# Kernel optimization log

Measured on AMD Instinct MI355X. Metric: run time of the kernel, lower is better.

## Reference

```python
import jax, jax.numpy as jnp
import numpy as np

INFEATURES = 4096
OUTFEATURES = 11008
GROUP_SIZE = 128
N_GROUPS = INFEATURES // GROUP_SIZE  # 32
PACK = 8  # 32 bits / 4 bits


def _unpack_int4(packed):
    # packed: [R, C//8] int32 -> [R, C] int32 nibbles in [0, 15]
    shifts = (jnp.arange(PACK, dtype=jnp.int32) * 4)
    nib = (packed[:, :, None] >> shifts[None, None, :]) & 0xF
    return nib.reshape(packed.shape[0], packed.shape[1] * PACK)


def setup_inputs() -> dict:
    key = jax.random.key(0)
    k1, k2, k3, k4, k5 = jax.random.split(key, 5)
    x = jax.random.normal(k1, (2048, INFEATURES), dtype=jnp.float32)
    qweight = jax.random.randint(k2, (INFEATURES, OUTFEATURES // PACK), 0, 2147483647, dtype=jnp.int32)
    qzeros = jax.random.randint(k3, (N_GROUPS, OUTFEATURES // PACK), 0, 2147483647, dtype=jnp.int32)
    scales = jax.random.uniform(k4, (N_GROUPS, OUTFEATURES), minval=0.001, maxval=0.01, dtype=jnp.float32)
    bias = jax.random.normal(k5, (OUTFEATURES,), dtype=jnp.float32) * 0.01
    return {"x": x, "qweight": qweight, "qzeros": qzeros, "scales": scales, "bias": bias}


def reference(x, qweight, qzeros, scales, bias):
    # convert_from_uint4: dequantize packed int4 weight with per-group scale/zero
    w_int = _unpack_int4(qweight)                       # [in, out] int4 values
    z_int = _unpack_int4(qzeros)                        # [n_groups, out]
    dt = scales.dtype
    # broadcast group params to per-row (trivial g_idx: row i -> group i // GROUP_SIZE)
    z = jnp.repeat(z_int.astype(dt), GROUP_SIZE, axis=0)      # [in, out]
    s = jnp.repeat(scales, GROUP_SIZE, axis=0)                # [in, out]
    weight = (w_int.astype(dt) - z) * s                       # [in, out]
    out = jnp.matmul(x, weight) + bias                        # [tokens, out]
    return out
```

## Files before the change

kernel.cpp:

```cpp
#include <hip/hip_runtime.h>

typedef __bf16 bf16_t;
typedef bf16_t bf16x8 __attribute__((ext_vector_type(8)));
typedef float  floatx4 __attribute__((ext_vector_type(4)));
typedef unsigned int uint;

constexpr int Mdim = 2048;
constexpr int Kdim = 4096;
constexpr int Ndim = 11008;
constexpr int NPK  = Ndim / 8;
constexpr int BM = 128, BN = 128, BK = 64;
constexpr int SA = 72;
constexpr int SB = 72;
constexpr int SQ = 68;

__global__ void xcast_kernel(const float* __restrict__ x, bf16_t* __restrict__ xb)
{
    const int i = (blockIdx.x * 256 + threadIdx.x) * 8;
    const float4 a = *(const float4*)(x + i);
    const float4 b = *(const float4*)(x + i + 4);
    bf16x8 v;
    v[0] = (bf16_t)a.x; v[1] = (bf16_t)a.y; v[2] = (bf16_t)a.z; v[3] = (bf16_t)a.w;
    v[4] = (bf16_t)b.x; v[5] = (bf16_t)b.y; v[6] = (bf16_t)b.z; v[7] = (bf16_t)b.w;
    *(bf16x8*)(xb + i) = v;
}

template <bool PRE>
__global__ __launch_bounds__(256, 3)
void qgemm_kernel(const float* __restrict__ x,
                  const bf16_t* __restrict__ xb,
                  const uint* __restrict__ qweight,
                  const uint* __restrict__ qzeros,
                  const float* __restrict__ scales,
                  const float* __restrict__ bias,
                  float* __restrict__ out)
{
    __shared__ bf16_t As[BM * SA];
    __shared__ bf16_t Bs[BN * SB];
    __shared__ uint   qbuf[16 * SQ];

    const int t  = threadIdx.x;
    const int m0 = blockIdx.y * BM;
    const int n0 = blockIdx.x * BN;
    const int c0 = n0 >> 3;

    const int wave = t >> 6;
    const int lane = t & 63;
    const int quad = lane >> 4;
    const int l16  = lane & 15;
    const int mw = (wave >> 1) * 64;
    const int nw = (wave & 1) * 64;

    floatx4 acc[4][4];
#pragma unroll
    for (int i = 0; i < 4; ++i)
#pragma unroll
        for (int j = 0; j < 4; ++j)
            acc[i][j] = (floatx4){0.f, 0.f, 0.f, 0.f};

    const int am = t >> 3;
    const int ao = t & 7;
    const int qk  = t >> 2;
    const int qc4 = (t & 3) * 4;
    const int nloc  = t & 127;
    const int khalf = t >> 7;
    const int cc    = nloc >> 3;
    const int jsh   = (nloc & 7) * 4;

    for (int kt = 0; kt < Kdim / BK; ++kt) {
        const int k0 = kt * BK;
        const int g  = k0 >> 7;

#pragma unroll
        for (int p = 0; p < 4; ++p) {
            const int m = p * 32 + am;
            if (PRE) {
                const bf16x8 v = *(const bf16x8*)(xb + (size_t)(m0 + m) * Kdim + k0 + ao * 8);
                *(bf16x8*)&As[m * SA + ao * 8] = v;
            } else {
                const float* src = x + (size_t)(m0 + m) * Kdim + k0 + ao * 8;
                const float4 a = *(const float4*)src;
                const float4 b = *(const float4*)(src + 4);
                bf16x8 v;
                v[0] = (bf16_t)a.x; v[1] = (bf16_t)a.y; v[2] = (bf16_t)a.z; v[3] = (bf16_t)a.w;
                v[4] = (bf16_t)b.x; v[5] = (bf16_t)b.y; v[6] = (bf16_t)b.z; v[7] = (bf16_t)b.w;
                *(bf16x8*)&As[m * SA + ao * 8] = v;
            }
        }
        {
            const uint4 w4 = *(const uint4*)(qweight + (size_t)(k0 + qk) * NPK + c0 + qc4);
            qbuf[(qc4 + 0) * SQ + qk] = w4.x;
            qbuf[(qc4 + 1) * SQ + qk] = w4.y;
            qbuf[(qc4 + 2) * SQ + qk] = w4.z;
            qbuf[(qc4 + 3) * SQ + qk] = w4.w;
        }
        __syncthreads();

        {
            const uint  zw = qzeros[(size_t)g * NPK + c0 + cc];
            const float s  = scales[(size_t)g * Ndim + n0 + nloc];
            const float zs = (float)((zw >> jsh) & 15u) * s;
            const uint* qrow = &qbuf[cc * SQ + khalf * 32];
#pragma unroll
            for (int j = 0; j < 4; ++j) {
                const uint4 qa = *(const uint4*)(qrow + j * 8);
                const uint4 qb = *(const uint4*)(qrow + j * 8 + 4);
                bf16x8 v;
                v[0] = (bf16_t)((float)((qa.x >> jsh) & 15u) * s - zs);
                v[1] = (bf16_t)((float)((qa.y >> jsh) & 15u) * s - zs);
                v[2] = (bf16_t)((float)((qa.z >> jsh) & 15u) * s - zs);
                v[3] = (bf16_t)((float)((qa.w >> jsh) & 15u) * s - zs);
                v[4] = (bf16_t)((float)((qb.x >> jsh) & 15u) * s - zs);
                v[5] = (bf16_t)((float)((qb.y >> jsh) & 15u) * s - zs);
                v[6] = (bf16_t)((float)((qb.z >> jsh) & 15u) * s - zs);
                v[7] = (bf16_t)((float)((qb.w >> jsh) & 15u) * s - zs);
                *(bf16x8*)&Bs[nloc * SB + khalf * 32 + j * 8] = v;
            }
        }
        __syncthreads();

#pragma unroll
        for (int s = 0; s < 2; ++s) {
            bf16x8 fa[4], fb[4];
#pragma unroll
            for (int mt = 0; mt < 4; ++mt)
                fa[mt] = *(const bf16x8*)&As[(mw + mt * 16 + l16) * SA + s * 32 + quad * 8];
#pragma unroll
            for (int nt = 0; nt < 4; ++nt)
                fb[nt] = *(const bf16x8*)&Bs[(nw + nt * 16 + l16) * SB + s * 32 + quad * 8];
#pragma unroll
            for (int mt = 0; mt < 4; ++mt)
#pragma unroll
                for (int nt = 0; nt < 4; ++nt)
                    acc[mt][nt] = __builtin_amdgcn_mfma_f32_16x16x32_bf16(fa[mt], fb[nt], acc[mt][nt], 0, 0, 0);
        }
        __syncthreads();
    }

#pragma unroll
    for (int nt = 0; nt < 4; ++nt) {
        const int col = n0 + nw + nt * 16 + l16;
        const float b = bias[col];
#pragma unroll
        for (int mt = 0; mt < 4; ++mt) {
#pragma unroll
            for (int r = 0; r < 4; ++r) {
                const int row = m0 + mw + mt * 16 + quad * 4 + r;
                out[(size_t)row * Ndim + col] = acc[mt][nt][r] + b;
            }
        }
    }
}

extern "C" void kernel_launch(void* const* d_in, const int* in_sizes, int n_in,
                              void* d_out, int out_size, void* d_ws, size_t ws_size,
                              hipStream_t stream)
{
    const float* x        = (const float*)d_in[0];
    const uint*  qweight  = (const uint*)d_in[1];
    const uint*  qzeros   = (const uint*)d_in[2];
    const float* scales   = (const float*)d_in[3];
    const float* bias     = (const float*)d_in[4];
    float*       out      = (float*)d_out;
    bf16_t*      xb       = (bf16_t*)d_ws;

    const size_t xb_bytes = (size_t)Mdim * Kdim * sizeof(bf16_t);
    dim3 grid(Ndim / BN, Mdim / BM);

    if (ws_size >= xb_bytes) {
        xcast_kernel<<<(Mdim * Kdim) / (256 * 8), 256, 0, stream>>>(x, xb);
        qgemm_kernel<true><<<grid, dim3(256), 0, stream>>>(x, xb, qweight, qzeros, scales, bias, out);
    } else {
        qgemm_kernel<false><<<grid, dim3(256), 0, stream>>>(x, xb, qweight, qzeros, scales, bias, out);
    }
}
```

Before: 398.8 us.

## Dequantize weights directly into MFMA fragments and load A via global_load_lds

Removes the Bs shared-memory tile: each wave now dequantizes int4 weights from the packed qbuf straight into B fragment registers, which drops one LDS store/load round trip and one barrier per K step. Scales and zeros are hoisted to once per 128-row group, with two 64-wide halves processed inside. The A tile is loaded with global_load_lds (direct global-to-LDS) into an XOR-swizzled unpadded layout to avoid bank conflicts. In exchange, dequant work is duplicated across the two waves that share each N slice, and register pressure rises.

```diff
diff --git a/kernel.cpp b/kernel.cpp
--- a/kernel.cpp
+++ b/kernel.cpp
@@ -10,8 +10,6 @@
 constexpr int Ndim = 11008;
 constexpr int NPK  = Ndim / 8;
 constexpr int BM = 128, BN = 128, BK = 64;
-constexpr int SA = 72;
-constexpr int SB = 72;
 constexpr int SQ = 68;
 
 __global__ void xcast_kernel(const float* __restrict__ x, bf16_t* __restrict__ xb)
@@ -23,6 +21,12 @@
     v[0] = (bf16_t)a.x; v[1] = (bf16_t)a.y; v[2] = (bf16_t)a.z; v[3] = (bf16_t)a.w;
     v[4] = (bf16_t)b.x; v[5] = (bf16_t)b.y; v[6] = (bf16_t)b.z; v[7] = (bf16_t)b.w;
     *(bf16x8*)(xb + i) = v;
+}
+
+__device__ __forceinline__ void gload_lds16(const bf16_t* g, bf16_t* l)
+{
+    __builtin_amdgcn_global_load_lds((const __attribute__((address_space(1))) void*)g,
+                                     (__attribute__((address_space(3))) void*)l, 16, 0, 0);
 }
 
 template <bool PRE>
@@ -35,8 +39,7 @@
                   const float* __restrict__ bias,
                   float* __restrict__ out)
 {
-    __shared__ bf16_t As[BM * SA];
-    __shared__ bf16_t Bs[BN * SB];
+    __shared__ bf16_t As[BM * BK];
     __shared__ uint   qbuf[16 * SQ];
 
     const int t  = threadIdx.x;
@@ -51,6 +54,30 @@
     const int mw = (wave >> 1) * 64;
     const int nw = (wave & 1) * 64;
 
+    const int r8   = lane >> 3;
+    const int gs   = lane & 7;
+    const int gcol = gs ^ r8;
+
+    const int qk  = t >> 2;
+    const int qc4 = (t & 3) * 4;
+
+    const int jsh = (l16 & 7) * 4;
+    const int e3  = l16 & 7;
+    int qrowoff[4];
+#pragma unroll
+    for (int nt = 0; nt < 4; ++nt)
+        qrowoff[nt] = ((nw >> 3) + nt * 2 + (l16 >> 3)) * SQ;
+    int arowoff[4];
+#pragma unroll
+    for (int mt = 0; mt < 4; ++mt)
+        arowoff[mt] = (mw + mt * 16 + l16) * BK;
+    int aslot[2], qoff[2];
+#pragma unroll
+    for (int s2 = 0; s2 < 2; ++s2) {
+        aslot[s2] = (((s2 * 4 + quad) ^ e3) * 8);
+        qoff[s2]  = s2 * 32 + quad * 8;
+    }
+
     floatx4 acc[4][4];
 #pragma unroll
     for (int i = 0; i < 4; ++i)
@@ -58,83 +85,81 @@
         for (int j = 0; j < 4; ++j)
             acc[i][j] = (floatx4){0.f, 0.f, 0.f, 0.f};
 
-    const int am = t >> 3;
-    const int ao = t & 7;
-    const int qk  = t >> 2;
-    const int qc4 = (t & 3) * 4;
-    const int nloc  = t & 127;
-    const int khalf = t >> 7;
-    const int cc    = nloc >> 3;
-    const int jsh   = (nloc & 7) * 4;
-
-    for (int kt = 0; kt < Kdim / BK; ++kt) {
-        const int k0 = kt * BK;
-        const int g  = k0 >> 7;
-
-#pragma unroll
-        for (int p = 0; p < 4; ++p) {
-            const int m = p * 32 + am;
+    for (int g = 0; g < 32; ++g) {
+        float sN[4], zsN[4];
+#pragma unroll
+        for (int nt = 0; nt < 4; ++nt) {
+            const int col = n0 + nw + nt * 16 + l16;
+            const float sv = scales[(size_t)g * Ndim + col];
+            const uint  zw = qzeros[(size_t)g * NPK + (col >> 3)];
+            sN[nt]  = sv;
+            zsN[nt] = (float)((zw >> jsh) & 15u) * sv;
+        }
+
+#pragma unroll 1
+        for (int half = 0; half < 2; ++half) {
+            const int k0 = g * 128 + half * 64;
+
             if (PRE) {
-                const bf16x8 v = *(const bf16x8*)(xb + (size_t)(m0 + m) * Kdim + k0 + ao * 8);
-                *(bf16x8*)&As[m * SA + ao * 8] = v;
+#pragma unroll
+                for (int p = 0; p < 4; ++p) {
+                    const bf16_t* gp = xb + (size_t)(m0 + p * 32 + wave * 8 + r8) * Kdim
+                                          + k0 + gcol * 8;
+                    gload_lds16(gp, &As[(p * 32 + wave * 8) * BK]);
+                }
             } else {
-                const float* src = x + (size_t)(m0 + m) * Kdim + k0 + ao * 8;
-                const float4 a = *(const float4*)src;
-                const float4 b = *(const float4*)(src + 4);
-                bf16x8 v;
-                v[0] = (bf16_t)a.x; v[1] = (bf16_t)a.y; v[2] = (bf16_t)a.z; v[3] = (bf16_t)a.w;
-                v[4] = (bf16_t)b.x; v[5] = (bf16_t)b.y; v[6] = (bf16_t)b.z; v[7] = (bf16_t)b.w;
-                *(bf16x8*)&As[m * SA + ao * 8] = v;
-            }
+#pragma unroll
+                for (int p = 0; p < 4; ++p) {
+                    const int row = p * 32 + wave * 8 + r8;
+                    const float* src = x + (size_t)(m0 + row) * Kdim + k0 + gcol * 8;
+                    const float4 a = *(const float4*)src;
+                    const float4 b = *(const float4*)(src + 4);
+                    bf16x8 v;
+                    v[0] = (bf16_t)a.x; v[1] = (bf16_t)a.y; v[2] = (bf16_t)a.z; v[3] = (bf16_t)a.w;
+                    v[4] = (bf16_t)b.x; v[5] = (bf16_t)b.y; v[6] = (bf16_t)b.z; v[7] = (bf16_t)b.w;
+                    *(bf16x8*)&As[row * BK + gs * 8] = v;
+                }
+            }
+
+            {
+                const uint4 w4 = *(const uint4*)(qweight + (size_t)(k0 + qk) * NPK + c0 + qc4);
+                qbuf[(qc4 + 0) * SQ + qk] = w4.x;
+                qbuf[(qc4 + 1) * SQ + qk] = w4.y;
+                qbuf[(qc4 + 2) * SQ + qk] = w4.z;
+                qbuf[(qc4 + 3) * SQ + qk] = w4.w;
+            }
+            __syncthreads();
+
+#pragma unroll
+            for (int s2 = 0; s2 < 2; ++s2) {
+                bf16x8 fa[4], fb[4];
+#pragma unroll
+                for (int mt = 0; mt < 4; ++mt)
+                    fa[mt] = *(const bf16x8*)&As[arowoff[mt] + aslot[s2]];
+#pragma unroll
+                for (int nt = 0; nt < 4; ++nt) {
+                    const uint* qr = &qbuf[qrowoff[nt] + qoff[s2]];
+                    const uint4 qa = *(const uint4*)qr;
+                    const uint4 qb = *(const uint4*)(qr + 4);
+                    bf16x8 v;
+                    v[0] = (bf16_t)((float)((qa.x >> jsh) & 15u) * sN[nt] - zsN[nt]);
+                    v[1] = (bf16_t)((float)((qa.y >> jsh) & 15u) * sN[nt] - zsN[nt]);
+                    v[2] = (bf16_t)((float)((qa.z >> jsh) & 15u) * sN[nt] - zsN[nt]);
+                    v[3] = (bf16_t)((float)((qa.w >> jsh) & 15u) * sN[nt] - zsN[nt]);
+                    v[4] = (bf16_t)((float)((qb.x >> jsh) & 15u) * sN[nt] - zsN[nt]);
+                    v[5] = (bf16_t)((float)((qb.y >> jsh) & 15u) * sN[nt] - zsN[nt]);
+                    v[6] = (bf16_t)((float)((qb.z >> jsh) & 15u) * sN[nt] - zsN[nt]);
+                    v[7] = (bf16_t)((float)((qb.w >> jsh) & 15u) * sN[nt] - zsN[nt]);
+                    fb[nt] = v;
+                }
+#pragma unroll
+                for (int mt = 0; mt < 4; ++mt)
+#pragma unroll
+                    for (int nt = 0; nt < 4; ++nt)
+                        acc[mt][nt] = __builtin_amdgcn_mfma_f32_16x16x32_bf16(fa[mt], fb[nt], acc[mt][nt], 0, 0, 0);
+            }
+            __syncthreads();
         }
-        {
-            const uint4 w4 = *(const uint4*)(qweight + (size_t)(k0 + qk) * NPK + c0 + qc4);
-            qbuf[(qc4 + 0) * SQ + qk] = w4.x;
-            qbuf[(qc4 + 1) * SQ + qk] = w4.y;
-            qbuf[(qc4 + 2) * SQ + qk] = w4.z;
-            qbuf[(qc4 + 3) * SQ + qk] = w4.w;
-        }
-        __syncthreads();
-
-        {
-            const uint  zw = qzeros[(size_t)g * NPK + c0 + cc];
-            const float s  = scales[(size_t)g * Ndim + n0 + nloc];
-            const float zs = (float)((zw >> jsh) & 15u) * s;
-            const uint* qrow = &qbuf[cc * SQ + khalf * 32];
-#pragma unroll
-            for (int j = 0; j < 4; ++j) {
-                const uint4 qa = *(const uint4*)(qrow + j * 8);
-                const uint4 qb = *(const uint4*)(qrow + j * 8 + 4);
-                bf16x8 v;
-                v[0] = (bf16_t)((float)((qa.x >> jsh) & 15u) * s - zs);
-                v[1] = (bf16_t)((float)((qa.y >> jsh) & 15u) * s - zs);
-                v[2] = (bf16_t)((float)((qa.z >> jsh) & 15u) * s - zs);
-                v[3] = (bf16_t)((float)((qa.w >> jsh) & 15u) * s - zs);
-                v[4] = (bf16_t)((float)((qb.x >> jsh) & 15u) * s - zs);
-                v[5] = (bf16_t)((float)((qb.y >> jsh) & 15u) * s - zs);
-                v[6] = (bf16_t)((float)((qb.z >> jsh) & 15u) * s - zs);
-                v[7] = (bf16_t)((float)((qb.w >> jsh) & 15u) * s - zs);
-                *(bf16x8*)&Bs[nloc * SB + khalf * 32 + j * 8] = v;
-            }
-        }
-        __syncthreads();
-
-#pragma unroll
-        for (int s = 0; s < 2; ++s) {
-            bf16x8 fa[4], fb[4];
-#pragma unroll
-            for (int mt = 0; mt < 4; ++mt)
-                fa[mt] = *(const bf16x8*)&As[(mw + mt * 16 + l16) * SA + s * 32 + quad * 8];
-#pragma unroll
-            for (int nt = 0; nt < 4; ++nt)
-                fb[nt] = *(const bf16x8*)&Bs[(nw + nt * 16 + l16) * SB + s * 32 + quad * 8];
-#pragma unroll
-            for (int mt = 0; mt < 4; ++mt)
-#pragma unroll
-                for (int nt = 0; nt < 4; ++nt)
-                    acc[mt][nt] = __builtin_amdgcn_mfma_f32_16x16x32_bf16(fa[mt], fb[nt], acc[mt][nt], 0, 0, 0);
-        }
-        __syncthreads();
     }
 
 #pragma unroll
@@ -156,13 +181,13 @@
                               void* d_out, int out_size, void* d_ws, size_t ws_size,
                               hipStream_t stream)
 {
-    const float* x        = (const float*)d_in[0];
-    const uint*  qweight  = (const uint*)d_in[1];
-    const uint*  qzeros   = (const uint*)d_in[2];
-    const float* scales   = (const float*)d_in[3];
-    const float* bias     = (const float*)d_in[4];
-    float*       out      = (float*)d_out;
-    bf16_t*      xb       = (bf16_t*)d_ws;
+    const float* x       = (const float*)d_in[0];
+    const uint*  qweight = (const uint*)d_in[1];
+    const uint*  qzeros  = (const uint*)d_in[2];
+    const float* scales  = (const float*)d_in[3];
+    const float* bias    = (const float*)d_in[4];
+    float*       out     = (float*)d_out;
+    bf16_t*      xb      = (bf16_t*)d_ws;
 
     const size_t xb_bytes = (size_t)Mdim * Kdim * sizeof(bf16_t);
     dim3 grid(Ndim / BN, Mdim / BM);
```

Measured after the change: 445.5 us. +11.7%, slower.
